# Kernel tuning notes

Measured on AMD Instinct MI355X. Metric: run time of the kernel, lower is better.

The kernel has to match this reference:

```python
import jax, jax.numpy as jnp
import numpy as np
from jax import lax

DIM = 256
HEAD_DIM = 64          # v head dim and hedgehog dim
HEAD_DIM_QK = 64       # must equal HEAD_DIM for the module to run
NH = DIM // HEAD_DIM   # 4
EPS = 1e-6


def setup_inputs() -> dict:
    key = jax.random.key(0)
    ks = jax.random.split(key, 12)
    B, C, H, W, D = 1, DIM, 16, 16, 16
    x = jax.random.normal(ks[0], (B, C, H, W, D), dtype=jnp.float32)
    qk_dim = HEAD_DIM_QK * NH
    # 1x1x1 conv weights for q, k (qkv_bias=False)
    Wq = jax.random.normal(ks[1], (qk_dim, C), dtype=jnp.float32) * 0.02
    Wk = jax.random.normal(ks[2], (qk_dim, C), dtype=jnp.float32) * 0.02
    # depthwise 3x3x3 conv for v (groups=dim, bias=True)
    Wv = jax.random.normal(ks[3], (C, 1, 3, 3, 3), dtype=jnp.float32) * 0.1
    bv = jax.random.normal(ks[4], (C,), dtype=jnp.float32) * 0.02
    # HedgeHog linear layers (init is identity/zeros; use near-identity + noise)
    eye = jnp.eye(HEAD_DIM, dtype=jnp.float32)
    Wmq = eye * 0.5 + jax.random.normal(ks[5], (HEAD_DIM, HEAD_DIM), dtype=jnp.float32) * 0.02
    bmq = jnp.zeros((HEAD_DIM,), dtype=jnp.float32)
    Wmk = eye * 0.5 + jax.random.normal(ks[6], (HEAD_DIM, HEAD_DIM), dtype=jnp.float32) * 0.02
    bmk = jnp.zeros((HEAD_DIM,), dtype=jnp.float32)
    Wmv = eye * 0.5 + jax.random.normal(ks[7], (HEAD_DIM, HEAD_DIM), dtype=jnp.float32) * 0.02
    bmv = jnp.zeros((HEAD_DIM,), dtype=jnp.float32)
    return {"x": x, "Wq": Wq, "Wk": Wk, "Wv": Wv, "bv": bv,
            "Wmq": Wmq, "bmq": bmq, "Wmk": Wmk, "bmk": bmk,
            "Wmv": Wmv, "bmv": bmv}


def _hedgehog(z, W, b):
    # z: [B, nh, N, d] -> [B, 2*nh, N, d]; cat along HEAD axis (dim=1) as in torch code
    h = jnp.einsum('bhnd,ed->bhne', z, W) + b
    return jnp.concatenate([jnp.exp(h), jnp.exp(-h)], axis=1)


def reference(x, Wq, Wk, Wv, bv, Wmq, bmq, Wmk, bmk, Wmv, bmv):
    B, C, H, W_, D = x.shape
    N = H * W_ * D
    x2 = x.reshape(B, C, N)
    # 1x1x1 conv projections
    q = jnp.einsum('oc,bcn->bon', Wq, x2)  # [B, qk_dim, N]
    k = jnp.einsum('oc,bcn->bon', Wk, x2)
    # depthwise 3x3x3 conv for v
    v3 = lax.conv_general_dilated(
        x, Wv, window_strides=(1, 1, 1),
        padding=((1, 1), (1, 1), (1, 1)),
        dimension_numbers=('NCDHW', 'OIDHW', 'NCDHW'),
        feature_group_count=C) + bv[None, :, None, None, None]
    v = v3.reshape(B, C, N)
    # split heads, tokens-last -> tokens axis
    q1 = q.reshape(B, NH, HEAD_DIM_QK, N).transpose(0, 1, 3, 2)  # [B,nh,N,dqk]
    k1 = k.reshape(B, NH, HEAD_DIM_QK, N).transpose(0, 1, 3, 2)
    v1 = v.reshape(B, NH, HEAD_DIM, N).transpose(0, 1, 3, 2)     # [B,nh,N,dv]
    qf = _hedgehog(q1, Wmq, bmq)  # [B,2nh,N,dqk]
    kf = _hedgehog(k1, Wmk, bmk)
    vf = _hedgehog(v1, Wmv, bmv)  # [B,2nh,N,dv]
    # quadratic "linear" attention: row-sum normalized QK^T
    qk = jnp.einsum('bhmd,bhnd->bhmn', qf, kf)          # [B,2nh,N,N]
    attn = qk / (jnp.sum(qk, axis=-1, keepdims=True) + EPS)
    out = jnp.einsum('bhmn,bhnd->bhmd', attn, vf)        # [B,2nh,N,dv]
    out = out.transpose(0, 1, 3, 2).reshape(B, 2 * C, H, W_, D)
    return out
```

## Files before the change

### kernel.cpp

```cpp
#include <hip/hip_runtime.h>
#include <math.h>

#define EPS_F 1e-6f

typedef __attribute__((ext_vector_type(8))) short bf16x8;
typedef __attribute__((ext_vector_type(4))) float f32x4;

#define OFF_BV  0
#define OFF_VC  (OFF_BV + 256)
#define OFF_PS  (OFF_VC + 256*4096)
#define OFF_PSV (OFF_PS + 8*64*4096)
#define OFF_SM  (OFF_PSV + 8*64*64)
#define OFF_SV  (OFF_SM + 8*4096)
#define OFF_QF  (OFF_SV + 512)
#define OFF_WQH (OFF_QF + 512*4096)
#define OFF_WQL (OFF_WQH + 32768)
#define OFF_WKH (OFF_WQL + 32768)
#define OFF_WKL (OFF_WKH + 32768)
#define OFF_XTH (OFF_WKL + 32768)
#define OFF_XTL (OFF_XTH + 524288)

__device__ __forceinline__ void split_bf16(float v, unsigned short& h, unsigned short& l) {
    unsigned int b = __float_as_uint(v);
    h = (unsigned short)(b >> 16);
    float fh = __uint_as_float(b & 0xFFFF0000u);
    l = (unsigned short)(__float_as_uint(v - fh) >> 16);
}

__global__ __launch_bounds__(256) void k_combine(
    const float* __restrict__ Wq, const float* __restrict__ Wk,
    const float* __restrict__ Wmq, const float* __restrict__ Wmk,
    const float* __restrict__ Wmv, const float* __restrict__ bmv,
    const float* __restrict__ bv, float* __restrict__ ws)
{
    int row = blockIdx.x;
    int c = threadIdx.x;
    int h = row >> 6, e = row & 63;
    float aq = 0.f, ak = 0.f;
    for (int d = 0; d < 64; ++d) {
        float mq = Wmq[e*64 + d];
        float mk = Wmk[e*64 + d];
        int src = (h*64 + d)*256 + c;
        aq = fmaf(mq, Wq[src], aq);
        ak = fmaf(mk, Wk[src], ak);
    }
    unsigned short hh, ll;
    unsigned short* WQH = (unsigned short*)(ws + OFF_WQH);
    unsigned short* WQL = (unsigned short*)(ws + OFF_WQL);
    unsigned short* WKH = (unsigned short*)(ws + OFF_WKH);
    unsigned short* WKL = (unsigned short*)(ws + OFF_WKL);
    split_bf16(aq, hh, ll); WQH[row*256 + c] = hh; WQL[row*256 + c] = ll;
    split_bf16(ak, hh, ll); WKH[row*256 + c] = hh; WKL[row*256 + c] = ll;
    if (c == 0) {
        float av = 0.f;
        for (int d = 0; d < 64; ++d) av = fmaf(Wmv[e*64 + d], bv[h*64 + d], av);
        ws[OFF_BV + row] = av + bmv[e];
    }
}

__global__ __launch_bounds__(256) void k_xt(
    const float* __restrict__ x, float* __restrict__ ws)
{
    __shared__ float Ts[64][65];
    int tx = blockIdx.x;
    int cy = blockIdx.y;
    int t = threadIdx.x;
    int lr = t >> 6, lc2 = t & 63;
    #pragma unroll
    for (int i = 0; i < 16; ++i) {
        int row = lr*16 + i;
        Ts[row][lc2] = x[(size_t)(cy*64 + row)*4096 + tx*64 + lc2];
    }
    __syncthreads();
    int tok = t >> 2, c16 = (t & 3) * 16;
    unsigned int hw[8], lw[8];
    #pragma unroll
    for (int j = 0; j < 8; ++j) {
        float v0 = Ts[c16 + 2*j][tok], v1 = Ts[c16 + 2*j + 1][tok];
        unsigned int b0 = __float_as_uint(v0), b1 = __float_as_uint(v1);
        hw[j] = (b0 >> 16) | (b1 & 0xFFFF0000u);
        float f0 = __uint_as_float(b0 & 0xFFFF0000u);
        float f1 = __uint_as_float(b1 & 0xFFFF0000u);
        lw[j] = (__float_as_uint(v0 - f0) >> 16) | (__float_as_uint(v1 - f1) & 0xFFFF0000u);
    }
    unsigned short* XH = (unsigned short*)(ws + OFF_XTH);
    unsigned short* XL = (unsigned short*)(ws + OFF_XTL);
    size_t base = (size_t)(tx*64 + tok)*256 + cy*64 + c16;
    uint4 H0 = {hw[0], hw[1], hw[2], hw[3]}, H1 = {hw[4], hw[5], hw[6], hw[7]};
    uint4 L0 = {lw[0], lw[1], lw[2], lw[3]}, L1 = {lw[4], lw[5], lw[6], lw[7]};
    *(uint4*)(XH + base) = H0;  *(uint4*)(XH + base + 8) = H1;
    *(uint4*)(XL + base) = L0;  *(uint4*)(XL + base + 8) = L1;
}

__global__ __launch_bounds__(256) void k_dwconv(
    const float* __restrict__ x, const float* __restrict__ Wv, float* __restrict__ vc)
{
    int c = blockIdx.y;
    int n = blockIdx.x * 256 + threadIdx.x;
    int z = n >> 8, y = (n >> 4) & 15, xx = n & 15;
    const float* xc = x + c * 4096;
    const float* wc = Wv + c * 27;
    float acc = 0.f;
    #pragma unroll
    for (int kz = 0; kz < 3; ++kz) {
        int zz = z + kz - 1;
        if (zz < 0 || zz > 15) continue;
        #pragma unroll
        for (int ky = 0; ky < 3; ++ky) {
            int yy = y + ky - 1;
            if (yy < 0 || yy > 15) continue;
            #pragma unroll
            for (int kx = 0; kx < 3; ++kx) {
                int xv = xx + kx - 1;
                if (xv < 0 || xv > 15) continue;
                acc = fmaf(wc[(kz*3 + ky)*3 + kx], xc[(zz << 8) + (yy << 4) + xv], acc);
            }
        }
    }
    vc[c*4096 + n] = acc;
}

__global__ __launch_bounds__(512, 2) void k_fused(
    const float* __restrict__ bmk, const float* __restrict__ bmq,
    const float* __restrict__ Wmv, float* __restrict__ ws)
{
    __shared__ float smem[16384];
    unsigned short* su = (unsigned short*)smem;

    int t = threadIdx.x;
    int chunk = blockIdx.x;
    int hb = blockIdx.y;
    int n0 = chunk * 64;
    int w = t >> 6, lane = t & 63;
    int kq = w >> 2;
    int mh = w & 1, nh = (w >> 1) & 1;
    int l15 = lane & 15, l4 = lane >> 4;
    bool isQ = (t >= 256);
    int tl = t & 255;
    int lc = tl >> 6, ln = tl & 63;
    int e4 = (tl & 15) * 4;
    int n4 = (tl >> 4) * 4;

    const unsigned short* XH  = (const unsigned short*)(ws + OFF_XTH);
    const unsigned short* XL  = (const unsigned short*)(ws + OFF_XTL);
    const unsigned short* WKHp = (const unsigned short*)(ws + OFF_WKH);
    const unsigned short* WKLp = (const unsigned short*)(ws + OFF_WKL);
    const unsigned short* WQHp = (const unsigned short*)(ws + OFF_WQH);
    const unsigned short* WQLp = (const unsigned short*)(ws + OFF_WQL);

    f32x4 acc[2][2];
    #pragma unroll
    for (int i = 0; i < 2; ++i)
        #pragma unroll
        for (int j = 0; j < 2; ++j) acc[i][j] = (f32x4){0.f, 0.f, 0.f, 0.f};
    float accV[4][4];
    #pragma unroll
    for (int i = 0; i < 4; ++i)
        #pragma unroll
        for (int j = 0; j < 4; ++j) accV[i][j] = 0.f;

    for (int cs = 0; cs < 4; ++cs) {
        int c0 = cs * 64;
        {
            int r = (t >> 3) & 63, s = t & 7;
            unsigned short* d = su + r*64 + (((s ^ (r & 7))) << 3);
            size_t xo = (size_t)(n0 + r)*256 + c0 + s*8;
            size_t wo = (size_t)(hb*64 + r)*256 + c0 + s*8;
            *(uint4*)(d)         = *(const uint4*)(XH + xo);
            *(uint4*)(d + 4096)  = *(const uint4*)(XL + xo);
            *(uint4*)(d + 8192)  = *(const uint4*)(WKHp + wo);
            *(uint4*)(d + 12288) = *(const uint4*)(WKLp + wo);
            *(uint4*)(d + 16384) = *(const uint4*)(WQHp + wo);
            *(uint4*)(d + 20480) = *(const uint4*)(WQLp + wo);
        }
        __syncthreads();
        const unsigned short* Xh = su;
        const unsigned short* Xl = su + 4096;
        const unsigned short* Wh = su + 8192 + kq*8192;
        const unsigned short* Wl = Wh + 4096;
        #pragma unroll
        for (int ks = 0; ks < 2; ++ks) {
            bf16x8 ah[2], al[2], bh_[2], bl_[2];
            #pragma unroll
            for (int mt = 0; mt < 2; ++mt) {
                int ar = mh*32 + mt*16 + l15;
                int off = ar*64 + (((ks*4 + l4) ^ (ar & 7)) << 3);
                ah[mt] = *(const bf16x8*)(Xh + off);
                al[mt] = *(const bf16x8*)(Xl + off);
            }
            #pragma unroll
            for (int nt = 0; nt < 2; ++nt) {
                int br = nh*32 + nt*16 + l15;
                int off = br*64 + (((ks*4 + l4) ^ (br & 7)) << 3);
                bh_[nt] = *(const bf16x8*)(Wh + off);
                bl_[nt] = *(const bf16x8*)(Wl + off);
            }
            #pragma unroll
            for (int mt = 0; mt < 2; ++mt)
                #pragma unroll
                for (int nt = 0; nt < 2; ++nt) {
                    acc[mt][nt] = __builtin_amdgcn_mfma_f32_16x16x32_bf16(ah[mt], bh_[nt], acc[mt][nt], 0, 0, 0);
                    acc[mt][nt] = __builtin_amdgcn_mfma_f32_16x16x32_bf16(al[mt], bh_[nt], acc[mt][nt], 0, 0, 0);
                    acc[mt][nt] = __builtin_amdgcn_mfma_f32_16x16x32_bf16(ah[mt], bl_[nt], acc[mt][nt], 0, 0, 0);
                }
        }
        __syncthreads();
    }

    float (*Xs)[64]  = (float(*)[64])smem;
    float (*Wsh)[68] = (float(*)[68])(smem + 4096);
    if (!isQ) {
        const float* vcb = ws + OFF_VC + (size_t)hb*64*4096;
        #pragma unroll
        for (int i = 0; i < 16; ++i)
            Xs[lc*16 + i][ln] = vcb[(size_t)(lc*16 + i)*4096 + n0 + ln];
        #pragma unroll
        for (int i = 0; i < 16; ++i) { int idx = i*256 + tl; Wsh[idx & 63][idx >> 6] = Wmv[idx]; }
    }
    __syncthreads();

    if (!isQ) {
        #pragma unroll 4
        for (int d = 0; d < 64; ++d) {
            float4 xv4 = *(const float4*)&Xs[d][n4];
            float4 wv4 = *(const float4*)&Wsh[d][e4];
            float xv[4] = {xv4.x, xv4.y, xv4.z, xv4.w};
            float wv[4] = {wv4.x, wv4.y, wv4.z, wv4.w};
            #pragma unroll
            for (int ii = 0; ii < 4; ++ii)
                #pragma unroll
                for (int jj = 0; jj < 4; ++jj)
                    accV[ii][jj] = fmaf(xv[ii], wv[jj], accV[ii][jj]);
        }
    }
    __syncthreads();

    float (*kfp)[64] = (float(*)[64])smem;
    float (*kfm)[64] = (float(*)[64])(smem + 4096);
    float (*vfp)[64] = (float(*)[64])(smem + 8192);
    float (*vfm)[64] = (float(*)[64])(smem + 12288);
    if (!isQ) {
        float bk0 = bmk[nh*32 + l15], bk1 = bmk[nh*32 + 16 + l15];
        #pragma unroll
        for (int mt = 0; mt < 2; ++mt)
            #pragma unroll
            for (int nt = 0; nt < 2; ++nt) {
                float bkv = nt ? bk1 : bk0;
                int feat = nh*32 + nt*16 + l15;
                #pragma unroll
                for (int r = 0; r < 4; ++r) {
                    int tok = mh*32 + mt*16 + l4*4 + r;
                    float v = acc[mt][nt][r] + bkv;
                    kfp[tok][feat] = __expf(v);
                    kfm[tok][feat] = __expf(-v);
                }
            }
        float bvv[4];
        #pragma unroll
        for (int j = 0; j < 4; ++j) bvv[j] = ws[OFF_BV + hb*64 + e4 + j];
        #pragma unroll
        for (int ii = 0; ii < 4; ++ii) {
            float pv[4], mv[4];
            #pragma unroll
            for (int jj = 0; jj < 4; ++jj) {
                float b = accV[ii][jj] + bvv[jj];
                pv[jj] = __expf(b);  mv[jj] = __expf(-b);
            }
            *(float4*)&vfp[n4 + ii][e4] = make_float4(pv[0], pv[1], pv[2], pv[3]);
            *(float4*)&vfm[n4 + ii][e4] = make_float4(mv[0], mv[1], mv[2], mv[3]);
        }
    }
    __syncthreads();

    float aSp[4][4], aSm[4][4], svp[4], svm[4];
    #pragma unroll
    for (int i = 0; i < 4; ++i) {
        svp[i] = 0.f; svm[i] = 0.f;
        #pragma unroll
        for (int j = 0; j < 4; ++j) { aSp[i][j] = 0.f; aSm[i][j] = 0.f; }
    }
    int a4 = e4, f4 = n4;
    int nb = isQ ? 32 : 0;
    #pragma unroll 2
    for (int nn = 0; nn < 32; ++nn) {
        int n = nb + nn;
        float4 kp4 = *(const float4*)&kfp[n][a4];
        float4 km4 = *(const float4*)&kfm[n][a4];
        float4 vp4 = *(const float4*)&vfp[n][f4];
        float4 vm4 = *(const float4*)&vfm[n][f4];
        float kp[4] = {kp4.x, kp4.y, kp4.z, kp4.w};
        float km[4] = {km4.x, km4.y, km4.z, km4.w};
        float vp[4] = {vp4.x, vp4.y, vp4.z, vp4.w};
        float vm[4] = {vm4.x, vm4.y, vm4.z, vm4.w};
        #pragma unroll
        for (int ai = 0; ai < 4; ++ai) {
            svp[ai] += kp[ai];  svm[ai] += km[ai];
            #pragma unroll
            for (int fi = 0; fi < 4; ++fi) {
                aSp[ai][fi] = fmaf(kp[ai], vp[fi], aSp[ai][fi]);
                aSm[ai][fi] = fmaf(km[ai], vm[fi], aSm[ai][fi]);
            }
        }
    }
    __syncthreads();

    if (isQ) {
        #pragma unroll
        for (int i = 0; i < 4; ++i)
            #pragma unroll
            for (int j = 0; j < 4; ++j) {
                smem[(i*4 + j)*256 + tl]      = aSp[i][j];
                smem[(16 + i*4 + j)*256 + tl] = aSm[i][j];
            }
        if (tl < 16) {
            #pragma unroll
            for (int i = 0; i < 4; ++i) {
                smem[8192 + i*16 + tl]      = svp[i];
                smem[8192 + 64 + i*16 + tl] = svm[i];
            }
        }
    }
    __syncthreads();
    if (!isQ) {
        #pragma unroll
        for (int i = 0; i < 4; ++i)
            #pragma unroll
            for (int j = 0; j < 4; ++j) {
                aSp[i][j] += smem[(i*4 + j)*256 + tl];
                aSm[i][j] += smem[(16 + i*4 + j)*256 + tl];
            }
        float* pSp = ws + OFF_PS + (size_t)(hb*64 + chunk)*4096;
        float* pSm = ws + OFF_PS + (size_t)((hb + 4)*64 + chunk)*4096;
        #pragma unroll
        for (int ai = 0; ai < 4; ++ai) {
            *(float4*)&pSp[(a4 + ai)*64 + f4] = make_float4(aSp[ai][0], aSp[ai][1], aSp[ai][2], aSp[ai][3]);
            *(float4*)&pSm[(a4 + ai)*64 + f4] = make_float4(aSm[ai][0], aSm[ai][1], aSm[ai][2], aSm[ai][3]);
        }
        if (tl < 16) {
            #pragma unroll
            for (int i = 0; i < 4; ++i) {
                svp[i] += smem[8192 + i*16 + tl];
                svm[i] += smem[8192 + 64 + i*16 + tl];
            }
            float* pvp = ws + OFF_PSV + (size_t)(hb*64 + chunk)*64;
            float* pvm = ws + OFF_PSV + (size_t)((hb + 4)*64 + chunk)*64;
            *(float4*)&pvp[a4] = make_float4(svp[0], svp[1], svp[2], svp[3]);
            *(float4*)&pvm[a4] = make_float4(svm[0], svm[1], svm[2], svm[3]);
        }
    }
    __syncthreads();

    float (*qTp)[68] = (float(*)[68])smem;
    float (*qTm)[68] = (float(*)[68])(smem + 4352);
    if (isQ) {
        float bq0 = bmq[nh*32 + l15], bq1 = bmq[nh*32 + 16 + l15];
        #pragma unroll
        for (int mt = 0; mt < 2; ++mt)
            #pragma unroll
            for (int nt = 0; nt < 2; ++nt) {
                float bqv = nt ? bq1 : bq0;
                int feat = nh*32 + nt*16 + l15;
                #pragma unroll
                for (int r = 0; r < 4; ++r) {
                    int tok = mh*32 + mt*16 + l4*4 + r;
                    float v = acc[mt][nt][r] + bqv;
                    qTp[feat][tok] = __expf(v);
                    qTm[feat][tok] = __expf(-v);
                }
            }
    }
    __syncthreads();
    float* gq = ws + OFF_QF;
    #pragma unroll
    for (int j = 0; j < 4; ++j) {
        int un = t + 512*j;
        int s = un >> 10;
        int rem = un & 1023;
        int feat = rem >> 4, t4 = (rem & 15) * 4;
        const float* src = (s ? &qTm[feat][t4] : &qTp[feat][t4]);
        float4 v = *(const float4*)src;
        *(float4*)&gq[(size_t)((hb + 4*s)*64 + feat)*4096 + n0 + t4] = v;
    }
}

__global__ __launch_bounds__(256) void k_reduce(float* __restrict__ ws)
{
    int idx = blockIdx.x*256 + threadIdx.x;
    if (idx < 8*4096) {
        int h = idx >> 12, r = idx & 4095;
        float s = 0.f;
        #pragma unroll 16
        for (int c = 0; c < 64; ++c) s += ws[OFF_PS + (size_t)(h*64 + c)*4096 + r];
        ws[OFF_SM + idx] = s;
    } else if (idx < 8*4096 + 512) {
        int j = idx - 8*4096;
        int h = j >> 6, e = j & 63;
        float s = 0.f;
        #pragma unroll 16
        for (int c = 0; c < 64; ++c) s += ws[OFF_PSV + (size_t)(h*64 + c)*64 + e];
        ws[OFF_SV + j] = s;
    }
}

__global__ __launch_bounds__(256, 2) void k_out(
    const float* __restrict__ ws, float* __restrict__ out)
{
    __shared__ float qs[64][64];
    __shared__ float Sms[64][64];
    __shared__ float svs[64];
    int t = threadIdx.x;
    int chunk = blockIdx.x;
    int h = blockIdx.y;
    int n0 = chunk * 64;
    int lc = t >> 6, ln = t & 63;

    const float* gq = ws + OFF_QF + (size_t)h*64*4096;
    #pragma unroll
    for (int i = 0; i < 16; ++i)
        qs[lc*16 + i][ln] = gq[(size_t)(lc*16 + i)*4096 + n0 + ln];
    const float* Smg = ws + OFF_SM + (size_t)h*4096;
    #pragma unroll
    for (int i = 0; i < 16; ++i) { int idx = i*256 + t; Sms[idx >> 6][idx & 63] = Smg[idx]; }
    if (t < 64) svs[t] = ws[OFF_SV + h*64 + t];
    __syncthreads();

    int n4 = (t & 15) * 4;
    int e4 = (t >> 4) * 4;
    float acc[4][4];
    float den[4] = {0.f, 0.f, 0.f, 0.f};
    #pragma unroll
    for (int i = 0; i < 4; ++i)
        #pragma unroll
        for (int j = 0; j < 4; ++j) acc[i][j] = 0.f;
    #pragma unroll 4
    for (int a = 0; a < 64; ++a) {
        float4 qv4 = *(const float4*)&qs[a][n4];
        float4 sm4 = *(const float4*)&Sms[a][e4];
        float qv[4] = {qv4.x, qv4.y, qv4.z, qv4.w};
        float sm[4] = {sm4.x, sm4.y, sm4.z, sm4.w};
        float sva = svs[a];
        #pragma unroll
        for (int nj = 0; nj < 4; ++nj) {
            den[nj] = fmaf(qv[nj], sva, den[nj]);
            #pragma unroll
            for (int ei = 0; ei < 4; ++ei)
                acc[ei][nj] = fmaf(sm[ei], qv[nj], acc[ei][nj]);
        }
    }
    float r[4];
    #pragma unroll
    for (int nj = 0; nj < 4; ++nj) r[nj] = 1.f / (den[nj] + EPS_F);
    #pragma unroll
    for (int ei = 0; ei < 4; ++ei)
        *(float4*)&out[(size_t)(h*64 + e4 + ei)*4096 + n0 + n4] =
            make_float4(acc[ei][0]*r[0], acc[ei][1]*r[1], acc[ei][2]*r[2], acc[ei][3]*r[3]);
}

extern "C" void kernel_launch(void* const* d_in, const int* in_sizes, int n_in,
                              void* d_out, int out_size, void* d_ws, size_t ws_size,
                              hipStream_t stream) {
    const float* x   = (const float*)d_in[0];
    const float* Wq  = (const float*)d_in[1];
    const float* Wk  = (const float*)d_in[2];
    const float* Wv  = (const float*)d_in[3];
    const float* bv  = (const float*)d_in[4];
    const float* Wmq = (const float*)d_in[5];
    const float* bmq = (const float*)d_in[6];
    const float* Wmk = (const float*)d_in[7];
    const float* bmk = (const float*)d_in[8];
    const float* Wmv = (const float*)d_in[9];
    const float* bmv = (const float*)d_in[10];
    float* out = (float*)d_out;
    float* ws  = (float*)d_ws;

    k_combine<<<256, 256, 0, stream>>>(Wq, Wk, Wmq, Wmk, Wmv, bmv, bv, ws);
    k_xt<<<dim3(64, 4), 256, 0, stream>>>(x, ws);
    k_dwconv<<<dim3(16, 256), 256, 0, stream>>>(x, Wv, ws + OFF_VC);
    k_fused<<<dim3(64, 4), 512, 0, stream>>>(bmk, bmq, Wmv, ws);
    k_reduce<<<130, 256, 0, stream>>>(ws);
    k_out<<<dim3(64, 8), 256, 0, stream>>>(ws, out);
}
```

Measured before the change: 133.2 us.

## Merge preprocessing kernels and halve token chunks to double block parallelism

```diff
diff --git a/kernel.cpp b/kernel.cpp
--- a/kernel.cpp
+++ b/kernel.cpp
@@ -9,8 +9,8 @@
 #define OFF_BV  0
 #define OFF_VC  (OFF_BV + 256)
 #define OFF_PS  (OFF_VC + 256*4096)
-#define OFF_PSV (OFF_PS + 8*64*4096)
-#define OFF_SM  (OFF_PSV + 8*64*64)
+#define OFF_PSV (OFF_PS + 8*128*4096)
+#define OFF_SM  (OFF_PSV + 8*128*64)
 #define OFF_SV  (OFF_SM + 8*4096)
 #define OFF_QF  (OFF_SV + 512)
 #define OFF_WQH (OFF_QF + 512*4096)
@@ -27,100 +27,98 @@
     l = (unsigned short)(__float_as_uint(v - fh) >> 16);
 }
 
-__global__ __launch_bounds__(256) void k_combine(
+__global__ __launch_bounds__(256) void k_pre(
+    const float* __restrict__ x,
     const float* __restrict__ Wq, const float* __restrict__ Wk,
+    const float* __restrict__ Wv, const float* __restrict__ bv,
     const float* __restrict__ Wmq, const float* __restrict__ Wmk,
     const float* __restrict__ Wmv, const float* __restrict__ bmv,
-    const float* __restrict__ bv, float* __restrict__ ws)
-{
-    int row = blockIdx.x;
-    int c = threadIdx.x;
-    int h = row >> 6, e = row & 63;
-    float aq = 0.f, ak = 0.f;
-    for (int d = 0; d < 64; ++d) {
-        float mq = Wmq[e*64 + d];
-        float mk = Wmk[e*64 + d];
-        int src = (h*64 + d)*256 + c;
-        aq = fmaf(mq, Wq[src], aq);
-        ak = fmaf(mk, Wk[src], ak);
-    }
-    unsigned short hh, ll;
-    unsigned short* WQH = (unsigned short*)(ws + OFF_WQH);
-    unsigned short* WQL = (unsigned short*)(ws + OFF_WQL);
-    unsigned short* WKH = (unsigned short*)(ws + OFF_WKH);
-    unsigned short* WKL = (unsigned short*)(ws + OFF_WKL);
-    split_bf16(aq, hh, ll); WQH[row*256 + c] = hh; WQL[row*256 + c] = ll;
-    split_bf16(ak, hh, ll); WKH[row*256 + c] = hh; WKL[row*256 + c] = ll;
-    if (c == 0) {
-        float av = 0.f;
-        for (int d = 0; d < 64; ++d) av = fmaf(Wmv[e*64 + d], bv[h*64 + d], av);
-        ws[OFF_BV + row] = av + bmv[e];
-    }
-}
-
-__global__ __launch_bounds__(256) void k_xt(
-    const float* __restrict__ x, float* __restrict__ ws)
+    float* __restrict__ ws)
 {
     __shared__ float Ts[64][65];
-    int tx = blockIdx.x;
-    int cy = blockIdx.y;
-    int t = threadIdx.x;
-    int lr = t >> 6, lc2 = t & 63;
-    #pragma unroll
-    for (int i = 0; i < 16; ++i) {
-        int row = lr*16 + i;
-        Ts[row][lc2] = x[(size_t)(cy*64 + row)*4096 + tx*64 + lc2];
-    }
-    __syncthreads();
-    int tok = t >> 2, c16 = (t & 3) * 16;
-    unsigned int hw[8], lw[8];
-    #pragma unroll
-    for (int j = 0; j < 8; ++j) {
-        float v0 = Ts[c16 + 2*j][tok], v1 = Ts[c16 + 2*j + 1][tok];
-        unsigned int b0 = __float_as_uint(v0), b1 = __float_as_uint(v1);
-        hw[j] = (b0 >> 16) | (b1 & 0xFFFF0000u);
-        float f0 = __uint_as_float(b0 & 0xFFFF0000u);
-        float f1 = __uint_as_float(b1 & 0xFFFF0000u);
-        lw[j] = (__float_as_uint(v0 - f0) >> 16) | (__float_as_uint(v1 - f1) & 0xFFFF0000u);
-    }
-    unsigned short* XH = (unsigned short*)(ws + OFF_XTH);
-    unsigned short* XL = (unsigned short*)(ws + OFF_XTL);
-    size_t base = (size_t)(tx*64 + tok)*256 + cy*64 + c16;
-    uint4 H0 = {hw[0], hw[1], hw[2], hw[3]}, H1 = {hw[4], hw[5], hw[6], hw[7]};
-    uint4 L0 = {lw[0], lw[1], lw[2], lw[3]}, L1 = {lw[4], lw[5], lw[6], lw[7]};
-    *(uint4*)(XH + base) = H0;  *(uint4*)(XH + base + 8) = H1;
-    *(uint4*)(XL + base) = L0;  *(uint4*)(XL + base + 8) = L1;
-}
-
-__global__ __launch_bounds__(256) void k_dwconv(
-    const float* __restrict__ x, const float* __restrict__ Wv, float* __restrict__ vc)
-{
-    int c = blockIdx.y;
-    int n = blockIdx.x * 256 + threadIdx.x;
-    int z = n >> 8, y = (n >> 4) & 15, xx = n & 15;
-    const float* xc = x + c * 4096;
-    const float* wc = Wv + c * 27;
-    float acc = 0.f;
-    #pragma unroll
-    for (int kz = 0; kz < 3; ++kz) {
-        int zz = z + kz - 1;
-        if (zz < 0 || zz > 15) continue;
-        #pragma unroll
-        for (int ky = 0; ky < 3; ++ky) {
-            int yy = y + ky - 1;
-            if (yy < 0 || yy > 15) continue;
-            #pragma unroll
-            for (int kx = 0; kx < 3; ++kx) {
-                int xv = xx + kx - 1;
-                if (xv < 0 || xv > 15) continue;
-                acc = fmaf(wc[(kz*3 + ky)*3 + kx], xc[(zz << 8) + (yy << 4) + xv], acc);
-            }
-        }
-    }
-    vc[c*4096 + n] = acc;
-}
-
-__global__ __launch_bounds__(512, 2) void k_fused(
+    int b = blockIdx.x, t = threadIdx.x;
+    if (b < 256) {
+        int row = b, c = t;
+        int h = row >> 6, e = row & 63;
+        float aq = 0.f, ak = 0.f;
+        for (int d = 0; d < 64; ++d) {
+            float mq = Wmq[e*64 + d];
+            float mk = Wmk[e*64 + d];
+            int src = (h*64 + d)*256 + c;
+            aq = fmaf(mq, Wq[src], aq);
+            ak = fmaf(mk, Wk[src], ak);
+        }
+        unsigned short hh, ll;
+        unsigned short* WQH = (unsigned short*)(ws + OFF_WQH);
+        unsigned short* WQL = (unsigned short*)(ws + OFF_WQL);
+        unsigned short* WKH = (unsigned short*)(ws + OFF_WKH);
+        unsigned short* WKL = (unsigned short*)(ws + OFF_WKL);
+        split_bf16(aq, hh, ll); WQH[row*256 + c] = hh; WQL[row*256 + c] = ll;
+        split_bf16(ak, hh, ll); WKH[row*256 + c] = hh; WKL[row*256 + c] = ll;
+        if (c == 0) {
+            float av = 0.f;
+            for (int d = 0; d < 64; ++d) av = fmaf(Wmv[e*64 + d], bv[h*64 + d], av);
+            ws[OFF_BV + row] = av + bmv[e];
+        }
+    } else if (b < 512) {
+        int bx = b - 256;
+        int tx = bx & 63, cy = bx >> 6;
+        int lr = t >> 6, lc2 = t & 63;
+        #pragma unroll
+        for (int i = 0; i < 16; ++i) {
+            int row = lr*16 + i;
+            Ts[row][lc2] = x[(size_t)(cy*64 + row)*4096 + tx*64 + lc2];
+        }
+        __syncthreads();
+        int tok = t >> 2, c16 = (t & 3) * 16;
+        unsigned int hw[8], lw[8];
+        #pragma unroll
+        for (int j = 0; j < 8; ++j) {
+            float v0 = Ts[c16 + 2*j][tok], v1 = Ts[c16 + 2*j + 1][tok];
+            unsigned int b0 = __float_as_uint(v0), b1 = __float_as_uint(v1);
+            hw[j] = (b0 >> 16) | (b1 & 0xFFFF0000u);
+            float f0 = __uint_as_float(b0 & 0xFFFF0000u);
+            float f1 = __uint_as_float(b1 & 0xFFFF0000u);
+            lw[j] = (__float_as_uint(v0 - f0) >> 16) | (__float_as_uint(v1 - f1) & 0xFFFF0000u);
+        }
+        unsigned short* XH = (unsigned short*)(ws + OFF_XTH);
+        unsigned short* XL = (unsigned short*)(ws + OFF_XTL);
+        size_t base = (size_t)(tx*64 + tok)*256 + cy*64 + c16;
+        uint4 H0 = {hw[0], hw[1], hw[2], hw[3]}, H1 = {hw[4], hw[5], hw[6], hw[7]};
+        uint4 L0 = {lw[0], lw[1], lw[2], lw[3]}, L1 = {lw[4], lw[5], lw[6], lw[7]};
+        *(uint4*)(XH + base) = H0;  *(uint4*)(XH + base + 8) = H1;
+        *(uint4*)(XL + base) = L0;  *(uint4*)(XL + base + 8) = L1;
+    } else {
+        int c = b - 512;
+        const float* xc = x + c * 4096;
+        const float* wc = Wv + c * 27;
+        #pragma unroll
+        for (int i = 0; i < 16; ++i) {
+            int n = t + 256*i;
+            int z = n >> 8, y = (n >> 4) & 15, xx = n & 15;
+            float acc = 0.f;
+            #pragma unroll
+            for (int kz = 0; kz < 3; ++kz) {
+                int zz = z + kz - 1;
+                if (zz < 0 || zz > 15) continue;
+                #pragma unroll
+                for (int ky = 0; ky < 3; ++ky) {
+                    int yy = y + ky - 1;
+                    if (yy < 0 || yy > 15) continue;
+                    #pragma unroll
+                    for (int kx = 0; kx < 3; ++kx) {
+                        int xv = xx + kx - 1;
+                        if (xv < 0 || xv > 15) continue;
+                        acc = fmaf(wc[(kz*3 + ky)*3 + kx], xc[(zz << 8) + (yy << 4) + xv], acc);
+                    }
+                }
+            }
+            ws[OFF_VC + (size_t)c*4096 + n] = acc;
+        }
+    }
+}
+
+__global__ __launch_bounds__(512, 4) void k_fused(
     const float* __restrict__ bmk, const float* __restrict__ bmq,
     const float* __restrict__ Wmv, float* __restrict__ ws)
 {
@@ -130,16 +128,14 @@
     int t = threadIdx.x;
     int chunk = blockIdx.x;
     int hb = blockIdx.y;
-    int n0 = chunk * 64;
+    int n0 = chunk * 32;
     int w = t >> 6, lane = t & 63;
     int kq = w >> 2;
-    int mh = w & 1, nh = (w >> 1) & 1;
+    int wi = w & 3;
+    int mh = wi & 1, nh = wi >> 1;
     int l15 = lane & 15, l4 = lane >> 4;
     bool isQ = (t >= 256);
     int tl = t & 255;
-    int lc = tl >> 6, ln = tl & 63;
-    int e4 = (tl & 15) * 4;
-    int n4 = (tl >> 4) * 4;
 
     const unsigned short* XH  = (const unsigned short*)(ws + OFF_XTH);
     const unsigned short* XL  = (const unsigned short*)(ws + OFF_XTL);
@@ -148,126 +144,120 @@
     const unsigned short* WQHp = (const unsigned short*)(ws + OFF_WQH);
     const unsigned short* WQLp = (const unsigned short*)(ws + OFF_WQL);
 
-    f32x4 acc[2][2];
+    f32x4 acc[2];
+    acc[0] = (f32x4){0.f, 0.f, 0.f, 0.f};
+    acc[1] = (f32x4){0.f, 0.f, 0.f, 0.f};
+    float accV[2][4];
     #pragma unroll
     for (int i = 0; i < 2; ++i)
-        #pragma unroll
-        for (int j = 0; j < 2; ++j) acc[i][j] = (f32x4){0.f, 0.f, 0.f, 0.f};
-    float accV[4][4];
-    #pragma unroll
-    for (int i = 0; i < 4; ++i)
         #pragma unroll
         for (int j = 0; j < 4; ++j) accV[i][j] = 0.f;
 
     for (int cs = 0; cs < 4; ++cs) {
         int c0 = cs * 64;
         {
-            int r = (t >> 3) & 63, s = t & 7;
-            unsigned short* d = su + r*64 + (((s ^ (r & 7))) << 3);
-            size_t xo = (size_t)(n0 + r)*256 + c0 + s*8;
-            size_t wo = (size_t)(hb*64 + r)*256 + c0 + s*8;
-            *(uint4*)(d)         = *(const uint4*)(XH + xo);
-            *(uint4*)(d + 4096)  = *(const uint4*)(XL + xo);
-            *(uint4*)(d + 8192)  = *(const uint4*)(WKHp + wo);
-            *(uint4*)(d + 12288) = *(const uint4*)(WKLp + wo);
-            *(uint4*)(d + 16384) = *(const uint4*)(WQHp + wo);
-            *(uint4*)(d + 20480) = *(const uint4*)(WQLp + wo);
+            int s = t & 7;
+            int xb = t >> 8;
+            int r5 = (t >> 3) & 31;
+            const unsigned short* XSrc = xb ? XL : XH;
+            unsigned short* xd = su + xb*2048 + r5*64 + (((s) ^ (r5 & 7)) << 3);
+            *(uint4*)xd = *(const uint4*)(XSrc + (size_t)(n0 + r5)*256 + c0 + s*8);
+            int r6 = (t >> 3) & 63;
+            size_t wo = (size_t)(hb*64 + r6)*256 + c0 + s*8;
+            unsigned short* wd0 = su + 4096 + r6*64 + (((s) ^ (r6 & 7)) << 3);
+            *(uint4*)(wd0)          = *(const uint4*)(WKHp + wo);
+            *(uint4*)(wd0 + 4096)   = *(const uint4*)(WKLp + wo);
+            *(uint4*)(wd0 + 8192)   = *(const uint4*)(WQHp + wo);
+            *(uint4*)(wd0 + 12288)  = *(const uint4*)(WQLp + wo);
         }
         __syncthreads();
         const unsigned short* Xh = su;
-        const unsigned short* Xl = su + 4096;
-        const unsigned short* Wh = su + 8192 + kq*8192;
+        const unsigned short* Xl = su + 2048;
+        const unsigned short* Wh = su + 4096 + kq*8192;
         const unsigned short* Wl = Wh + 4096;
         #pragma unroll
         for (int ks = 0; ks < 2; ++ks) {
-            bf16x8 ah[2], al[2], bh_[2], bl_[2];
-            #pragma unroll
-            for (int mt = 0; mt < 2; ++mt) {
-                int ar = mh*32 + mt*16 + l15;
-                int off = ar*64 + (((ks*4 + l4) ^ (ar & 7)) << 3);
-                ah[mt] = *(const bf16x8*)(Xh + off);
-                al[mt] = *(const bf16x8*)(Xl + off);
-            }
+            int ar = mh*16 + l15;
+            int aoff = ar*64 + (((ks*4 + l4) ^ (ar & 7)) << 3);
+            bf16x8 ah = *(const bf16x8*)(Xh + aoff);
+            bf16x8 al = *(const bf16x8*)(Xl + aoff);
             #pragma unroll
             for (int nt = 0; nt < 2; ++nt) {
                 int br = nh*32 + nt*16 + l15;
-                int off = br*64 + (((ks*4 + l4) ^ (br & 7)) << 3);
-                bh_[nt] = *(const bf16x8*)(Wh + off);
-                bl_[nt] = *(const bf16x8*)(Wl + off);
-            }
-            #pragma unroll
-            for (int mt = 0; mt < 2; ++mt)
-                #pragma unroll
-                for (int nt = 0; nt < 2; ++nt) {
-                    acc[mt][nt] = __builtin_amdgcn_mfma_f32_16x16x32_bf16(ah[mt], bh_[nt], acc[mt][nt], 0, 0, 0);
-                    acc[mt][nt] = __builtin_amdgcn_mfma_f32_16x16x32_bf16(al[mt], bh_[nt], acc[mt][nt], 0, 0, 0);
-                    acc[mt][nt] = __builtin_amdgcn_mfma_f32_16x16x32_bf16(ah[mt], bl_[nt], acc[mt][nt], 0, 0, 0);
-                }
+                int boff = br*64 + (((ks*4 + l4) ^ (br & 7)) << 3);
+                bf16x8 bh = *(const bf16x8*)(Wh + boff);
+                bf16x8 bl = *(const bf16x8*)(Wl + boff);
+                acc[nt] = __builtin_amdgcn_mfma_f32_16x16x32_bf16(ah, bh, acc[nt], 0, 0, 0);
+                acc[nt] = __builtin_amdgcn_mfma_f32_16x16x32_bf16(al, bh, acc[nt], 0, 0, 0);
+                acc[nt] = __builtin_amdgcn_mfma_f32_16x16x32_bf16(ah, bl, acc[nt], 0, 0, 0);
+            }
         }
         __syncthreads();
     }
 
-    float (*Xs)[64]  = (float(*)[64])smem;
-    float (*Wsh)[68] = (float(*)[68])(smem + 4096);
+    float* Vs = smem + 8192;
+    float* Wms = smem + 10240;
     if (!isQ) {
         const float* vcb = ws + OFF_VC + (size_t)hb*64*4096;
         #pragma unroll
-        for (int i = 0; i < 16; ++i)
-            Xs[lc*16 + i][ln] = vcb[(size_t)(lc*16 + i)*4096 + n0 + ln];
-        #pragma unroll
-        for (int i = 0; i < 16; ++i) { int idx = i*256 + tl; Wsh[idx & 63][idx >> 6] = Wmv[idx]; }
-    }
-    __syncthreads();
-
+        for (int i = 0; i < 8; ++i) {
+            int idx = i*256 + tl;
+            int row = idx >> 5, col = idx & 31;
+            Vs[row*32 + col] = vcb[(size_t)row*4096 + n0 + col];
+        }
+        #pragma unroll
+        for (int i = 0; i < 16; ++i) { int idx = i*256 + tl; Wms[(idx & 63)*68 + (idx >> 6)] = Wmv[idx]; }
+    }
+    __syncthreads();
+
+    int n2 = (tl >> 4) * 2;
+    int e4 = (tl & 15) * 4;
     if (!isQ) {
         #pragma unroll 4
         for (int d = 0; d < 64; ++d) {
-            float4 xv4 = *(const float4*)&Xs[d][n4];
-            float4 wv4 = *(const float4*)&Wsh[d][e4];
-            float xv[4] = {xv4.x, xv4.y, xv4.z, xv4.w};
+            float x0 = Vs[d*32 + n2], x1 = Vs[d*32 + n2 + 1];
+            float4 wv4 = *(const float4*)&Wms[d*68 + e4];
             float wv[4] = {wv4.x, wv4.y, wv4.z, wv4.w};
             #pragma unroll
-            for (int ii = 0; ii < 4; ++ii)
-                #pragma unroll
-                for (int jj = 0; jj < 4; ++jj)
-                    accV[ii][jj] = fmaf(xv[ii], wv[jj], accV[ii][jj]);
-        }
-    }
-    __syncthreads();
-
-    float (*kfp)[64] = (float(*)[64])smem;
-    float (*kfm)[64] = (float(*)[64])(smem + 4096);
-    float (*vfp)[64] = (float(*)[64])(smem + 8192);
-    float (*vfm)[64] = (float(*)[64])(smem + 12288);
+            for (int jj = 0; jj < 4; ++jj) {
+                accV[0][jj] = fmaf(x0, wv[jj], accV[0][jj]);
+                accV[1][jj] = fmaf(x1, wv[jj], accV[1][jj]);
+            }
+        }
+    }
+    __syncthreads();
+
+    float* kfp = smem;
+    float* kfm = smem + 2048;
+    float* vfp = smem + 4096;
+    float* vfm = smem + 6144;
     if (!isQ) {
         float bk0 = bmk[nh*32 + l15], bk1 = bmk[nh*32 + 16 + l15];
         #pragma unroll
-        for (int mt = 0; mt < 2; ++mt)
-            #pragma unroll
-            for (int nt = 0; nt < 2; ++nt) {
-                float bkv = nt ? bk1 : bk0;
-                int feat = nh*32 + nt*16 + l15;
-                #pragma unroll
-                for (int r = 0; r < 4; ++r) {
-                    int tok = mh*32 + mt*16 + l4*4 + r;
-                    float v = acc[mt][nt][r] + bkv;
-                    kfp[tok][feat] = __expf(v);
-                    kfm[tok][feat] = __expf(-v);
-                }
-            }
+        for (int nt = 0; nt < 2; ++nt) {
+            float bkv = nt ? bk1 : bk0;
+            int feat = nh*32 + nt*16 + l15;
+            #pragma unroll
+            for (int r = 0; r < 4; ++r) {
+                int tok = mh*16 + l4*4 + r;
+                float v = acc[nt][r] + bkv;
+                kfp[tok*64 + feat] = __expf(v);
+                kfm[tok*64 + feat] = __expf(-v);
+            }
+        }
         float bvv[4];
         #pragma unroll
         for (int j = 0; j < 4; ++j) bvv[j] = ws[OFF_BV + hb*64 + e4 + j];
         #pragma unroll
-        for (int ii = 0; ii < 4; ++ii) {
+        for (int ii = 0; ii < 2; ++ii) {
             float pv[4], mv[4];
             #pragma unroll
             for (int jj = 0; jj < 4; ++jj) {
-                float b = accV[ii][jj] + bvv[jj];
-                pv[jj] = __expf(b);  mv[jj] = __expf(-b);
-            }
-            *(float4*)&vfp[n4 + ii][e4] = make_float4(pv[0], pv[1], pv[2], pv[3]);
-            *(float4*)&vfm[n4 + ii][e4] = make_float4(mv[0], mv[1], mv[2], mv[3]);
+                float bb = accV[ii][jj] + bvv[jj];
+                pv[jj] = __expf(bb);  mv[jj] = __expf(-bb);
+            }
+            *(float4*)&vfp[(n2 + ii)*64 + e4] = make_float4(pv[0], pv[1], pv[2], pv[3]);
+            *(float4*)&vfm[(n2 + ii)*64 + e4] = make_float4(mv[0], mv[1], mv[2], mv[3]);
         }
     }
     __syncthreads();
@@ -279,15 +269,15 @@
         #pragma unroll
         for (int j = 0; j < 4; ++j) { aSp[i][j] = 0.f; aSm[i][j] = 0.f; }
     }
-    int a4 = e4, f4 = n4;
-    int nb = isQ ? 32 : 0;
+    int a4 = (tl & 15) * 4, f4 = (tl >> 4) * 4;
+    int nb = isQ ? 16 : 0;
     #pragma unroll 2
-    for (int nn = 0; nn < 32; ++nn) {
+    for (int nn = 0; nn < 16; ++nn) {
         int n = nb + nn;
-        float4 kp4 = *(const float4*)&kfp[n][a4];
-        float4 km4 = *(const float4*)&kfm[n][a4];
-        float4 vp4 = *(const float4*)&vfp[n][f4];
-        float4 vm4 = *(const float4*)&vfm[n][f4];
+        float4 kp4 = *(const float4*)&kfp[n*64 + a4];
+        float4 km4 = *(const float4*)&kfm[n*64 + a4];
+        float4 vp4 = *(const float4*)&vfp[n*64 + f4];
+        float4 vm4 = *(const float4*)&vfm[n*64 + f4];
         float kp[4] = {kp4.x, kp4.y, kp4.z, kp4.w};
         float km[4] = {km4.x, km4.y, km4.z, km4.w};
         float vp[4] = {vp4.x, vp4.y, vp4.z, vp4.w};
@@ -329,8 +319,8 @@
                 aSp[i][j] += smem[(i*4 + j)*256 + tl];
                 aSm[i][j] += smem[(16 + i*4 + j)*256 + tl];
             }
-        float* pSp = ws + OFF_PS + (size_t)(hb*64 + chunk)*4096;
-        float* pSm = ws + OFF_PS + (size_t)((hb + 4)*64 + chunk)*4096;
+        float* pSp = ws + OFF_PS + (size_t)(hb*128 + chunk)*4096;
+        float* pSm = ws + OFF_PS + (size_t)((hb + 4)*128 + chunk)*4096;
         #pragma unroll
         for (int ai = 0; ai < 4; ++ai) {
             *(float4*)&pSp[(a4 + ai)*64 + f4] = make_float4(aSp[ai][0], aSp[ai][1], aSp[ai][2], aSp[ai][3]);
@@ -342,42 +332,40 @@
                 svp[i] += smem[8192 + i*16 + tl];
                 svm[i] += smem[8192 + 64 + i*16 + tl];
             }
-            float* pvp = ws + OFF_PSV + (size_t)(hb*64 + chunk)*64;
-            float* pvm = ws + OFF_PSV + (size_t)((hb + 4)*64 + chunk)*64;
+            float* pvp = ws + OFF_PSV + (size_t)(hb*128 + chunk)*64;
+            float* pvm = ws + OFF_PSV + (size_t)((hb + 4)*128 + chunk)*64;
             *(float4*)&pvp[a4] = make_float4(svp[0], svp[1], svp[2], svp[3]);
             *(float4*)&pvm[a4] = make_float4(svm[0], svm[1], svm[2], svm[3]);
         }
     }
     __syncthreads();
 
-    float (*qTp)[68] = (float(*)[68])smem;
-    float (*qTm)[68] = (float(*)[68])(smem + 4352);
+    float* qTp = smem;
+    float* qTm = smem + 2304;
     if (isQ) {
         float bq0 = bmq[nh*32 + l15], bq1 = bmq[nh*32 + 16 + l15];
         #pragma unroll
-        for (int mt = 0; mt < 2; ++mt)
-            #pragma unroll
-            for (int nt = 0; nt < 2; ++nt) {
-                float bqv = nt ? bq1 : bq0;
-                int feat = nh*32 + nt*16 + l15;
-                #pragma unroll
-                for (int r = 0; r < 4; ++r) {
-                    int tok = mh*32 + mt*16 + l4*4 + r;
-                    float v = acc[mt][nt][r] + bqv;
-                    qTp[feat][tok] = __expf(v);
-                    qTm[feat][tok] = __expf(-v);
-                }
-            }
+        for (int nt = 0; nt < 2; ++nt) {
+            float bqv = nt ? bq1 : bq0;
+            int feat = nh*32 + nt*16 + l15;
+            #pragma unroll
+            for (int r = 0; r < 4; ++r) {
+                int tok = mh*16 + l4*4 + r;
+                float v = acc[nt][r] + bqv;
+                qTp[feat*36 + tok] = __expf(v);
+                qTm[feat*36 + tok] = __expf(-v);
+            }
+        }
     }
     __syncthreads();
     float* gq = ws + OFF_QF;
     #pragma unroll
-    for (int j = 0; j < 4; ++j) {
+    for (int j = 0; j < 2; ++j) {
         int un = t + 512*j;
-        int s = un >> 10;
-        int rem = un & 1023;
-        int feat = rem >> 4, t4 = (rem & 15) * 4;
-        const float* src = (s ? &qTm[feat][t4] : &qTp[feat][t4]);
+        int s = un >> 9;
+        int rem = un & 511;
+        int feat = rem >> 3, t4 = (rem & 7) * 4;
+        const float* src = (s ? &qTm[feat*36 + t4] : &qTp[feat*36 + t4]);
         float4 v = *(const float4*)src;
         *(float4*)&gq[(size_t)((hb + 4*s)*64 + feat)*4096 + n0 + t4] = v;
     }
@@ -390,69 +378,68 @@
         int h = idx >> 12, r = idx & 4095;
         float s = 0.f;
         #pragma unroll 16
-        for (int c = 0; c < 64; ++c) s += ws[OFF_PS + (size_t)(h*64 + c)*4096 + r];
+        for (int c = 0; c < 128; ++c) s += ws[OFF_PS + (size_t)(h*128 + c)*4096 + r];
         ws[OFF_SM + idx] = s;
     } else if (idx < 8*4096 + 512) {
         int j = idx - 8*4096;
         int h = j >> 6, e = j & 63;
         float s = 0.f;
         #pragma unroll 16
-        for (int c = 0; c < 64; ++c) s += ws[OFF_PSV + (size_t)(h*64 + c)*64 + e];
+        for (int c = 0; c < 128; ++c) s += ws[OFF_PSV + (size_t)(h*128 + c)*64 + e];
         ws[OFF_SV + j] = s;
     }
 }
 
-__global__ __launch_bounds__(256, 2) void k_out(
+__global__ __launch_bounds__(256, 4) void k_out(
     const float* __restrict__ ws, float* __restrict__ out)
 {
-    __shared__ float qs[64][64];
+    __shared__ float qs[64][32];
     __shared__ float Sms[64][64];
     __shared__ float svs[64];
     int t = threadIdx.x;
-    int chunk = blockIdx.x;
+    int cx = blockIdx.x;
     int h = blockIdx.y;
-    int n0 = chunk * 64;
-    int lc = t >> 6, ln = t & 63;
+    int n0 = cx * 32;
 
     const float* gq = ws + OFF_QF + (size_t)h*64*4096;
     #pragma unroll
-    for (int i = 0; i < 16; ++i)
-        qs[lc*16 + i][ln] = gq[(size_t)(lc*16 + i)*4096 + n0 + ln];
+    for (int i = 0; i < 8; ++i) {
+        int idx = i*256 + t;
+        qs[idx >> 5][idx & 31] = gq[(size_t)(idx >> 5)*4096 + n0 + (idx & 31)];
+    }
     const float* Smg = ws + OFF_SM + (size_t)h*4096;
     #pragma unroll
     for (int i = 0; i < 16; ++i) { int idx = i*256 + t; Sms[idx >> 6][idx & 63] = Smg[idx]; }
     if (t < 64) svs[t] = ws[OFF_SV + h*64 + t];
     __syncthreads();
 
-    int n4 = (t & 15) * 4;
-    int e4 = (t >> 4) * 4;
-    float acc[4][4];
+    int e2 = (t >> 3) * 2;
+    int n4 = (t & 7) * 4;
+    float acc[2][4];
     float den[4] = {0.f, 0.f, 0.f, 0.f};
     #pragma unroll
-    for (int i = 0; i < 4; ++i)
+    for (int i = 0; i < 2; ++i)
         #pragma unroll
         for (int j = 0; j < 4; ++j) acc[i][j] = 0.f;
     #pragma unroll 4
     for (int a = 0; a < 64; ++a) {
         float4 qv4 = *(const float4*)&qs[a][n4];
-        float4 sm4 = *(const float4*)&Sms[a][e4];
         float qv[4] = {qv4.x, qv4.y, qv4.z, qv4.w};
-        float sm[4] = {sm4.x, sm4.y, sm4.z, sm4.w};
+        float sm0 = Sms[a][e2], sm1 = Sms[a][e2 + 1];
         float sva = svs[a];
         #pragma unroll
         for (int nj = 0; nj < 4; ++nj) {
             den[nj] = fmaf(qv[nj], sva, den[nj]);
-            #pragma unroll
-            for (int ei = 0; ei < 4; ++ei)
-                acc[ei][nj] = fmaf(sm[ei], qv[nj], acc[ei][nj]);
+            acc[0][nj] = fmaf(sm0, qv[nj], acc[0][nj]);
+            acc[1][nj] = fmaf(sm1, qv[nj], acc[1][nj]);
         }
     }
     float r[4];
     #pragma unroll
     for (int nj = 0; nj < 4; ++nj) r[nj] = 1.f / (den[nj] + EPS_F);
     #pragma unroll
-    for (int ei = 0; ei < 4; ++ei)
-        *(float4*)&out[(size_t)(h*64 + e4 + ei)*4096 + n0 + n4] =
+    for (int ei = 0; ei < 2; ++ei)
+        *(float4*)&out[(size_t)(h*64 + e2 + ei)*4096 + n0 + n4] =
             make_float4(acc[ei][0]*r[0], acc[ei][1]*r[1], acc[ei][2]*r[2], acc[ei][3]*r[3]);
 }
 
@@ -473,10 +460,8 @@
     float* out = (float*)d_out;
     float* ws  = (float*)d_ws;
 
-    k_combine<<<256, 256, 0, stream>>>(Wq, Wk, Wmq, Wmk, Wmv, bmv, bv, ws);
-    k_xt<<<dim3(64, 4), 256, 0, stream>>>(x, ws);
-    k_dwconv<<<dim3(16, 256), 256, 0, stream>>>(x, Wv, ws + OFF_VC);
-    k_fused<<<dim3(64, 4), 512, 0, stream>>>(bmk, bmq, Wmv, ws);
+    k_pre<<<768, 256, 0, stream>>>(x, Wq, Wk, Wv, bv, Wmq, Wmk, Wmv, bmv, ws);
+    k_fused<<<dim3(128, 4), 512, 0, stream>>>(bmk, bmq, Wmv, ws);
     k_reduce<<<130, 256, 0, stream>>>(ws);
-    k_out<<<dim3(64, 8), 256, 0, stream>>>(ws, out);
-}
+    k_out<<<dim3(128, 8), 256, 0, stream>>>(ws, out);
+}
```

New measurement: 155.9 us. 1.17x slower.
